# Kernel tuning notes

Hardware: AMD Instinct MI355X
Metric: run time of the kernel (lower is better)

Reference implementation:

```python
import jax, jax.numpy as jnp
import numpy as np

B, C, H, W = 16, 64, 128, 128
BN_EPS = 1e-5


def setup_inputs() -> dict:
    key = jax.random.key(0)
    ks = jax.random.split(key, 8)
    inp = {
        "x1": jax.random.normal(ks[0], (B, C, H, W), dtype=jnp.float32),
        "x2": jax.random.normal(ks[1], (B, C, H, W), dtype=jnp.float32),
        "rssi1": jax.random.normal(ks[2], (B, C, H, W), dtype=jnp.float32),
        "rssi2": jax.random.normal(ks[3], (B, C, H, W), dtype=jnp.float32),
        # 1x1 conv weights == per-pixel channel matmul; trunc_normal(std=0.02) approximated by normal*0.02
        "q_w": jax.random.normal(ks[4], (C, C), dtype=jnp.float32) * 0.02,
        "q_b": jnp.zeros((C,), dtype=jnp.float32),
        "k_w": jax.random.normal(ks[5], (C, C), dtype=jnp.float32) * 0.02,
        "k_b": jnp.zeros((C,), dtype=jnp.float32),
        "v_w": jax.random.normal(ks[6], (C, C), dtype=jnp.float32) * 0.02,
        "v_b": jnp.zeros((C,), dtype=jnp.float32),
        "bn_gamma": jnp.ones((C,), dtype=jnp.float32),
        "bn_beta": jnp.zeros((C,), dtype=jnp.float32),
    }
    return inp


def _proj(w, b, x):
    # 1x1 Conv2d: contract channel dim
    return jnp.einsum('oc,bchw->bohw', w, x) + b[None, :, None, None]


def _branch(q_w, q_b, k_w, k_b, v_w, v_b, rssi, x):
    q = _proj(q_w, q_b, rssi)            # [B,C,H,W]
    k = _proj(k_w, k_b, x)               # [B,C,H,W]
    v = _proj(v_w, v_b, x)               # [B,C,H,W]
    scale = 1.0 / jnp.sqrt(jnp.asarray(k.shape[-2], dtype=q.dtype))
    # matmul over trailing dims: [B,C,H,W] @ [B,C,W,H] -> [B,C,H,H]
    score = jax.nn.softmax(jnp.einsum('bchw,bcgw->bchg', q, k) * scale, axis=-1)
    return jnp.einsum('bchg,bcgw->bchw', score, v)  # [B,C,H,W]


def reference(x1, x2, rssi1, rssi2, q_w, q_b, k_w, k_b, v_w, v_b, bn_gamma, bn_beta):
    csi1 = _branch(q_w, q_b, k_w, k_b, v_w, v_b, rssi1, x1)
    csi2 = _branch(q_w, q_b, k_w, k_b, v_w, v_b, rssi2, x2)
    fused = csi1 + csi2
    # BatchNorm2d (training mode -> batch statistics over B,H,W), then ReLU
    mean = jnp.mean(fused, axis=(0, 2, 3), keepdims=True)
    var = jnp.var(fused, axis=(0, 2, 3), keepdims=True)
    g = bn_gamma[None, :, None, None]
    b = bn_beta[None, :, None, None]
    normed = (fused - mean) * jax.lax.rsqrt(var + BN_EPS) * g + b
    return jax.nn.relu(normed)
```

## Files before the change

### kernel.cpp

```cpp
#include <hip/hip_runtime.h>

#define HW 16384
#define NE 16777216ull

typedef short bf16x8 __attribute__((ext_vector_type(8)));
typedef _Float16 f16x8 __attribute__((ext_vector_type(8)));
typedef float f32x4  __attribute__((ext_vector_type(4)));

__device__ __forceinline__ unsigned short f2bf(float f) {
    unsigned int u = __float_as_uint(f);
    unsigned int r = (u + 0x7FFFu + ((u >> 16) & 1u)) >> 16;
    return (unsigned short)r;
}

__global__ __launch_bounds__(256)
void proj_mfma_kernel(const float* __restrict__ in,
                      const float* __restrict__ w1, const float* __restrict__ b1,
                      unsigned short* __restrict__ out1,
                      const float* __restrict__ w2, const float* __restrict__ b2,
                      unsigned short* __restrict__ out2,
                      float* __restrict__ stats) {
    __shared__ __align__(16) _Float16 xT[256 * 64];
    unsigned short* obuf = reinterpret_cast<unsigned short*>(xT);
    int tid = threadIdx.x;
    if (stats != nullptr && blockIdx.x == 0 && tid < 128) stats[tid] = 0.f;
    int pbase = blockIdx.x * 256;
    int b = pbase >> 14;
    int hw0 = pbase & 16383;
    const float* inb = in + (size_t)b * (64 * HW);

    {
        int n = tid;
        int swz = n & 7;
        const float* colp = inb + hw0 + n;
#pragma unroll
        for (int kc = 0; kc < 8; ++kc) {
            f16x8 ev;
#pragma unroll
            for (int j = 0; j < 8; ++j)
                ev[j] = (_Float16)colp[(kc * 8 + j) * HW];
            *reinterpret_cast<f16x8*>(&xT[n * 64 + ((kc ^ swz) * 8)]) = ev;
        }
    }

    int lane = tid & 63;
    int wv = tid >> 6;
    int quad = lane >> 4;
    int m16 = lane & 15;
    int mb = wv * 16;
    int sw = m16 & 7;
    int hasw2 = (w2 != nullptr);

    f16x8 a1[2], a2[2];
    float bias1[4], bias2[4];
#pragma unroll
    for (int ks = 0; ks < 2; ++ks) {
        const float* wr = w1 + (mb + m16) * 64 + (ks * 4 + quad) * 8;
        f16x8 ev;
#pragma unroll
        for (int j = 0; j < 8; ++j) ev[j] = (_Float16)wr[j];
        a1[ks] = ev;
    }
#pragma unroll
    for (int r = 0; r < 4; ++r) bias1[r] = b1[mb + quad * 4 + r];
    if (hasw2) {
#pragma unroll
        for (int ks = 0; ks < 2; ++ks) {
            const float* wr = w2 + (mb + m16) * 64 + (ks * 4 + quad) * 8;
            f16x8 ev;
#pragma unroll
            for (int j = 0; j < 8; ++j) ev[j] = (_Float16)wr[j];
            a2[ks] = ev;
        }
#pragma unroll
        for (int r = 0; r < 4; ++r) bias2[r] = b2[mb + quad * 4 + r];
    }
    __syncthreads();

    unsigned short* o1 = out1 + (size_t)b * (64 * HW);
    unsigned short* o2 = hasw2 ? (out2 + (size_t)b * (64 * HW)) : out1;

    unsigned int pk1[32], pk2[32];
#pragma unroll
    for (int nt = 0; nt < 16; ++nt) {
        int row = nt * 16 + m16;
        f16x8 bF0 = *reinterpret_cast<const f16x8*>(&xT[row * 64 + ((quad ^ sw) * 8)]);
        f16x8 bF1 = *reinterpret_cast<const f16x8*>(&xT[row * 64 + (((4 + quad) ^ sw) * 8)]);
        f32x4 acc1 = {bias1[0], bias1[1], bias1[2], bias1[3]};
        acc1 = __builtin_amdgcn_mfma_f32_16x16x32_f16(a1[0], bF0, acc1, 0, 0, 0);
        acc1 = __builtin_amdgcn_mfma_f32_16x16x32_f16(a1[1], bF1, acc1, 0, 0, 0);
        pk1[nt * 2 + 0] = (unsigned int)f2bf(acc1[0]) | ((unsigned int)f2bf(acc1[1]) << 16);
        pk1[nt * 2 + 1] = (unsigned int)f2bf(acc1[2]) | ((unsigned int)f2bf(acc1[3]) << 16);
        if (hasw2) {
            f32x4 acc2 = {bias2[0], bias2[1], bias2[2], bias2[3]};
            acc2 = __builtin_amdgcn_mfma_f32_16x16x32_f16(a2[0], bF0, acc2, 0, 0, 0);
            acc2 = __builtin_amdgcn_mfma_f32_16x16x32_f16(a2[1], bF1, acc2, 0, 0, 0);
            pk2[nt * 2 + 0] = (unsigned int)f2bf(acc2[0]) | ((unsigned int)f2bf(acc2[1]) << 16);
            pk2[nt * 2 + 1] = (unsigned int)f2bf(acc2[2]) | ((unsigned int)f2bf(acc2[3]) << 16);
        }
    }
    __syncthreads();

#pragma unroll
    for (int nt = 0; nt < 16; ++nt)
#pragma unroll
        for (int r = 0; r < 4; ++r) {
            int row = mb + quad * 4 + r;
            int col = nt * 16 + m16;
            unsigned int v = pk1[nt * 2 + (r >> 1)];
            unsigned short e = (r & 1) ? (unsigned short)(v >> 16) : (unsigned short)(v & 0xffff);
            obuf[row * 256 + (((col >> 3) ^ (row & 7)) * 8) + (col & 7)] = e;
        }
    __syncthreads();
#pragma unroll
    for (int k = 0; k < 8; ++k) {
        int c = k * 256 + tid;
        int row = c >> 5;
        int cg = c & 31;
        uint4 v = *reinterpret_cast<const uint4*>(&obuf[row * 256 + ((cg ^ (row & 7)) * 8)]);
        *reinterpret_cast<uint4*>(&o1[(size_t)row * HW + hw0 + cg * 8]) = v;
    }

    if (hasw2) {
        __syncthreads();
#pragma unroll
        for (int nt = 0; nt < 16; ++nt)
#pragma unroll
            for (int r = 0; r < 4; ++r) {
                int row = mb + quad * 4 + r;
                int col = nt * 16 + m16;
                unsigned int v = pk2[nt * 2 + (r >> 1)];
                unsigned short e = (r & 1) ? (unsigned short)(v >> 16) : (unsigned short)(v & 0xffff);
                obuf[row * 256 + (((col >> 3) ^ (row & 7)) * 8) + (col & 7)] = e;
            }
        __syncthreads();
#pragma unroll
        for (int k = 0; k < 8; ++k) {
            int c = k * 256 + tid;
            int row = c >> 5;
            int cg = c & 31;
            uint4 v = *reinterpret_cast<const uint4*>(&obuf[row * 256 + ((cg ^ (row & 7)) * 8)]);
            *reinterpret_cast<uint4*>(&o2[(size_t)row * HW + hw0 + cg * 8]) = v;
        }
    }
}

__global__ __launch_bounds__(512, 4)
void attn_kernel(const unsigned short* __restrict__ Q, const unsigned short* __restrict__ K,
                 const unsigned short* __restrict__ V, float* __restrict__ io,
                 float* __restrict__ stats, int accumulate) {
    __shared__ short bufA[16384];
    __shared__ short bufB[16384];
    int bc = blockIdx.x;
    size_t base = (size_t)bc * HW;
    int tid = threadIdx.x;
    int lane = tid & 63;
    int wv = tid >> 6;
    int quad = lane >> 4;
    int m16 = lane & 15;

    uint4 vreg[4];
    {
        int g0 = tid >> 4;
        int w0 = (tid & 15) * 8;
#pragma unroll
        for (int i = 0; i < 4; ++i)
            vreg[i] = *(const uint4*)(V + base + (size_t)(g0 + 32 * i) * 128 + w0);
    }

    {
        int r0 = tid >> 4;
        int c0 = tid & 15;
#pragma unroll
        for (int i = 0; i < 4; ++i) {
            int r = r0 + 32 * i;
            uint4 q = *(const uint4*)(Q + base + (size_t)r * 128 + c0 * 8);
            uint4 k = *(const uint4*)(K + base + (size_t)r * 128 + c0 * 8);
            int ch = c0 ^ (r & 7);
            *reinterpret_cast<uint4*>(&bufA[r * 128 + ch * 8]) = q;
            *reinterpret_cast<uint4*>(&bufB[r * 128 + ch * 8]) = k;
        }
    }
    __syncthreads();

    int rowA = wv * 16 + m16;
    int sw = m16 & 7;
    bf16x8 aF[4];
#pragma unroll
    for (int ks = 0; ks < 4; ++ks) {
        int ch = (ks * 4 + quad) ^ sw;
        aF[ks] = *reinterpret_cast<const bf16x8*>(&bufA[rowA * 128 + ch * 8]);
    }
    f32x4 sacc[8];
#pragma unroll
    for (int n = 0; n < 8; ++n) {
        f32x4 acc = {0.f, 0.f, 0.f, 0.f};
        int rowB = n * 16 + m16;
#pragma unroll
        for (int ks = 0; ks < 4; ++ks) {
            int ch = (ks * 4 + quad) ^ sw;
            bf16x8 bF = *reinterpret_cast<const bf16x8*>(&bufB[rowB * 128 + ch * 8]);
            acc = __builtin_amdgcn_mfma_f32_16x16x32_bf16(aF[ks], bF, acc, 0, 0, 0);
        }
        sacc[n] = acc;
    }

    const float scale = 0.08838834764831845f;
    float mx[4] = {-3.4e38f, -3.4e38f, -3.4e38f, -3.4e38f};
#pragma unroll
    for (int n = 0; n < 8; ++n)
#pragma unroll
        for (int r = 0; r < 4; ++r) {
            sacc[n][r] *= scale;
            mx[r] = fmaxf(mx[r], sacc[n][r]);
        }
#pragma unroll
    for (int mask = 8; mask >= 1; mask >>= 1)
#pragma unroll
        for (int r = 0; r < 4; ++r) mx[r] = fmaxf(mx[r], __shfl_xor(mx[r], mask));
    float sum[4] = {0.f, 0.f, 0.f, 0.f};
#pragma unroll
    for (int n = 0; n < 8; ++n)
#pragma unroll
        for (int r = 0; r < 4; ++r) {
            float e = __expf(sacc[n][r] - mx[r]);
            sacc[n][r] = e;
            sum[r] += e;
        }
#pragma unroll
    for (int mask = 8; mask >= 1; mask >>= 1)
#pragma unroll
        for (int r = 0; r < 4; ++r) sum[r] += __shfl_xor(sum[r], mask);
    float inv[4];
#pragma unroll
    for (int r = 0; r < 4; ++r) inv[r] = 1.0f / sum[r];

#pragma unroll
    for (int n = 0; n < 8; ++n)
#pragma unroll
        for (int r = 0; r < 4; ++r) {
            int row = wv * 16 + quad * 4 + r;
            int col = n * 16 + m16;
            int pos = row * 128 + (((col >> 3) ^ (row & 7)) * 8) + (col & 7);
            bufA[pos] = (short)f2bf(sacc[n][r] * inv[r]);
        }

    __syncthreads();

    float iopre[8][4];
    if (accumulate) {
#pragma unroll
        for (int n = 0; n < 8; ++n)
#pragma unroll
            for (int r = 0; r < 4; ++r)
                iopre[n][r] = io[base + (wv * 16 + quad * 4 + r) * 128 + n * 16 + m16];
    }

    {
        int g0 = tid >> 4;
        int w0 = (tid & 15) * 8;
#pragma unroll
        for (int i = 0; i < 4; ++i) {
            int g = g0 + 32 * i;
            unsigned short e[8];
            *(uint4*)e = vreg[i];
#pragma unroll
            for (int jj = 0; jj < 8; ++jj) {
                int j = jj ^ (tid & 7);
                int w = w0 + j;
                int pos = w * 128 + (((g >> 3) ^ (w & 7)) * 8) + (g & 7);
                bufB[pos] = (short)e[j];
            }
        }
    }
    __syncthreads();

#pragma unroll
    for (int ks = 0; ks < 4; ++ks) {
        int ch = (ks * 4 + quad) ^ sw;
        aF[ks] = *reinterpret_cast<const bf16x8*>(&bufA[rowA * 128 + ch * 8]);
    }
    f32x4 oacc[8];
#pragma unroll
    for (int n = 0; n < 8; ++n) {
        f32x4 acc = {0.f, 0.f, 0.f, 0.f};
        int rowB = n * 16 + m16;
#pragma unroll
        for (int ks = 0; ks < 4; ++ks) {
            int ch = (ks * 4 + quad) ^ sw;
            bf16x8 bF = *reinterpret_cast<const bf16x8*>(&bufB[rowB * 128 + ch * 8]);
            acc = __builtin_amdgcn_mfma_f32_16x16x32_bf16(aF[ks], bF, acc, 0, 0, 0);
        }
        oacc[n] = acc;
    }

    if (!accumulate) {
#pragma unroll
        for (int n = 0; n < 8; ++n)
#pragma unroll
            for (int r = 0; r < 4; ++r) {
                int row = wv * 16 + quad * 4 + r;
                int col = n * 16 + m16;
                io[base + row * 128 + col] = oacc[n][r];
            }
    } else {
        float lsum = 0.f, lsq = 0.f;
#pragma unroll
        for (int n = 0; n < 8; ++n)
#pragma unroll
            for (int r = 0; r < 4; ++r) {
                int row = wv * 16 + quad * 4 + r;
                int col = n * 16 + m16;
                size_t idx = base + row * 128 + col;
                float f = iopre[n][r] + oacc[n][r];
                io[idx] = f;
                lsum += f;
                lsq += f * f;
            }
#pragma unroll
        for (int mask = 32; mask >= 1; mask >>= 1) {
            lsum += __shfl_xor(lsum, mask);
            lsq  += __shfl_xor(lsq,  mask);
        }
        if (lane == 0) {
            int c = bc & 63;
            atomicAdd(&stats[c], lsum);
            atomicAdd(&stats[64 + c], lsq);
        }
    }
}

__global__ __launch_bounds__(256)
void bn_relu_kernel(float* __restrict__ io, const float* __restrict__ stats,
                    const float* __restrict__ gamma, const float* __restrict__ beta) {
    int idx = blockIdx.x * 256 + threadIdx.x;
    int e = idx << 2;
    int c = (e >> 14) & 63;
    const float invN = 1.0f / 262144.0f;
    float mean = stats[c] * invN;
    float var = stats[64 + c] * invN - mean * mean;
    float k = rsqrtf(var + 1e-5f) * gamma[c];
    float bb = beta[c] - mean * k;
    float4 f = reinterpret_cast<const float4*>(io)[idx];
    float4 o;
    o.x = fmaxf(f.x * k + bb, 0.f);
    o.y = fmaxf(f.y * k + bb, 0.f);
    o.z = fmaxf(f.z * k + bb, 0.f);
    o.w = fmaxf(f.w * k + bb, 0.f);
    reinterpret_cast<float4*>(io)[idx] = o;
}

extern "C" void kernel_launch(void* const* d_in, const int* in_sizes, int n_in,
                              void* d_out, int out_size, void* d_ws, size_t ws_size,
                              hipStream_t stream) {
    const float* x1 = (const float*)d_in[0];
    const float* x2 = (const float*)d_in[1];
    const float* rssi1 = (const float*)d_in[2];
    const float* rssi2 = (const float*)d_in[3];
    const float* qw = (const float*)d_in[4];
    const float* qb = (const float*)d_in[5];
    const float* kw = (const float*)d_in[6];
    const float* kb = (const float*)d_in[7];
    const float* vw = (const float*)d_in[8];
    const float* vb = (const float*)d_in[9];
    const float* gamma = (const float*)d_in[10];
    const float* beta = (const float*)d_in[11];

    float* stats = (float*)d_ws;
    unsigned short* Q = (unsigned short*)((char*)d_ws + 512);
    unsigned short* K = Q + NE;
    unsigned short* V = K + NE;
    float* io = (float*)d_out;

    proj_mfma_kernel<<<1024, 256, 0, stream>>>(rssi1, qw, qb, Q,
                                               nullptr, nullptr, nullptr, stats);
    proj_mfma_kernel<<<1024, 256, 0, stream>>>(x1, kw, kb, K, vw, vb, V, nullptr);
    attn_kernel<<<1024, 512, 0, stream>>>(Q, K, V, io, stats, 0);

    proj_mfma_kernel<<<1024, 256, 0, stream>>>(rssi2, qw, qb, Q,
                                               nullptr, nullptr, nullptr, nullptr);
    proj_mfma_kernel<<<1024, 256, 0, stream>>>(x2, kw, kb, K, vw, vb, V, nullptr);
    attn_kernel<<<1024, 512, 0, stream>>>(Q, K, V, io, stats, 1);

    bn_relu_kernel<<<16384, 256, 0, stream>>>(io, stats, gamma, beta);
}
```

Before: 443.5 us.

## Fuse both branches into single projection and attention launches

Merges the four projection launches into one grid that picks its job from the block index. When the workspace is large enough, the two attention passes become one kernel that computes both branches and accumulates them in registers. This removes the read-modify-write of the fp32 output between branches and cuts launch count. Q fragments are now loaded straight from global memory instead of staged through shared memory. The cost is a larger workspace, more register pressure in the attention kernel, and extra synchronisation inside it.

```diff
diff --git a/kernel.cpp b/kernel.cpp
--- a/kernel.cpp
+++ b/kernel.cpp
@@ -14,17 +14,30 @@
 }
 
 __global__ __launch_bounds__(256)
-void proj_mfma_kernel(const float* __restrict__ in,
-                      const float* __restrict__ w1, const float* __restrict__ b1,
-                      unsigned short* __restrict__ out1,
-                      const float* __restrict__ w2, const float* __restrict__ b2,
-                      unsigned short* __restrict__ out2,
+void proj_mfma_kernel(const float* __restrict__ rA, const float* __restrict__ xA,
+                      const float* __restrict__ rB, const float* __restrict__ xB,
+                      const float* __restrict__ qw, const float* __restrict__ qb,
+                      const float* __restrict__ kw, const float* __restrict__ kb,
+                      const float* __restrict__ vw, const float* __restrict__ vb,
+                      unsigned short* __restrict__ QA, unsigned short* __restrict__ KA,
+                      unsigned short* __restrict__ VA,
+                      unsigned short* __restrict__ QB, unsigned short* __restrict__ KB,
+                      unsigned short* __restrict__ VB,
                       float* __restrict__ stats) {
     __shared__ __align__(16) _Float16 xT[256 * 64];
     unsigned short* obuf = reinterpret_cast<unsigned short*>(xT);
     int tid = threadIdx.x;
     if (stats != nullptr && blockIdx.x == 0 && tid < 128) stats[tid] = 0.f;
-    int pbase = blockIdx.x * 256;
+
+    int job = blockIdx.x >> 10;
+    const float *in, *w1, *b1, *w2 = nullptr, *b2 = nullptr;
+    unsigned short *o1, *o2 = nullptr;
+    if (job == 0)      { in = rA; w1 = qw; b1 = qb; o1 = QA; }
+    else if (job == 1) { in = xA; w1 = kw; b1 = kb; o1 = KA; w2 = vw; b2 = vb; o2 = VA; }
+    else if (job == 2) { in = rB; w1 = qw; b1 = qb; o1 = QB; }
+    else               { in = xB; w1 = kw; b1 = kb; o1 = KB; w2 = vw; b2 = vb; o2 = VB; }
+
+    int pbase = (blockIdx.x & 1023) * 256;
     int b = pbase >> 14;
     int hw0 = pbase & 16383;
     const float* inb = in + (size_t)b * (64 * HW);
@@ -77,8 +90,8 @@
     }
     __syncthreads();
 
-    unsigned short* o1 = out1 + (size_t)b * (64 * HW);
-    unsigned short* o2 = hasw2 ? (out2 + (size_t)b * (64 * HW)) : out1;
+    unsigned short* o1b = o1 + (size_t)b * (64 * HW);
+    unsigned short* o2b = hasw2 ? (o2 + (size_t)b * (64 * HW)) : o1b;
 
     unsigned int pk1[32], pk2[32];
 #pragma unroll
@@ -118,7 +131,7 @@
         int row = c >> 5;
         int cg = c & 31;
         uint4 v = *reinterpret_cast<const uint4*>(&obuf[row * 256 + ((cg ^ (row & 7)) * 8)]);
-        *reinterpret_cast<uint4*>(&o1[(size_t)row * HW + hw0 + cg * 8]) = v;
+        *reinterpret_cast<uint4*>(&o1b[(size_t)row * HW + hw0 + cg * 8]) = v;
     }
 
     if (hasw2) {
@@ -140,16 +153,18 @@
             int row = c >> 5;
             int cg = c & 31;
             uint4 v = *reinterpret_cast<const uint4*>(&obuf[row * 256 + ((cg ^ (row & 7)) * 8)]);
-            *reinterpret_cast<uint4*>(&o2[(size_t)row * HW + hw0 + cg * 8]) = v;
+            *reinterpret_cast<uint4*>(&o2b[(size_t)row * HW + hw0 + cg * 8]) = v;
         }
     }
 }
 
 __global__ __launch_bounds__(512, 4)
-void attn_kernel(const unsigned short* __restrict__ Q, const unsigned short* __restrict__ K,
-                 const unsigned short* __restrict__ V, float* __restrict__ io,
-                 float* __restrict__ stats, int accumulate) {
-    __shared__ short bufA[16384];
+void attn_kernel(const unsigned short* __restrict__ Q1, const unsigned short* __restrict__ K1,
+                 const unsigned short* __restrict__ V1,
+                 const unsigned short* __restrict__ Q2, const unsigned short* __restrict__ K2,
+                 const unsigned short* __restrict__ V2,
+                 float* __restrict__ io, float* __restrict__ stats, int mode) {
+    __shared__ short bufP[16384];
     __shared__ short bufB[16384];
     int bc = blockIdx.x;
     size_t base = (size_t)bc * HW;
@@ -158,39 +173,33 @@
     int wv = tid >> 6;
     int quad = lane >> 4;
     int m16 = lane & 15;
-
-    uint4 vreg[4];
-    {
-        int g0 = tid >> 4;
-        int w0 = (tid & 15) * 8;
-#pragma unroll
-        for (int i = 0; i < 4; ++i)
-            vreg[i] = *(const uint4*)(V + base + (size_t)(g0 + 32 * i) * 128 + w0);
-    }
-
-    {
-        int r0 = tid >> 4;
-        int c0 = tid & 15;
-#pragma unroll
-        for (int i = 0; i < 4; ++i) {
-            int r = r0 + 32 * i;
-            uint4 q = *(const uint4*)(Q + base + (size_t)r * 128 + c0 * 8);
-            uint4 k = *(const uint4*)(K + base + (size_t)r * 128 + c0 * 8);
-            int ch = c0 ^ (r & 7);
-            *reinterpret_cast<uint4*>(&bufA[r * 128 + ch * 8]) = q;
-            *reinterpret_cast<uint4*>(&bufB[r * 128 + ch * 8]) = k;
-        }
-    }
-    __syncthreads();
-
     int rowA = wv * 16 + m16;
     int sw = m16 & 7;
+    int g0 = tid >> 4;
+    int c0 = tid & 15;
+    int w0 = c0 * 8;
+
+    uint4 vreg[4];
+#pragma unroll
+    for (int i = 0; i < 4; ++i)
+        vreg[i] = *(const uint4*)(V1 + base + (size_t)(g0 + 32 * i) * 128 + w0);
+    uint4 kst[4];
+#pragma unroll
+    for (int i = 0; i < 4; ++i)
+        kst[i] = *(const uint4*)(K1 + base + (size_t)(g0 + 32 * i) * 128 + w0);
     bf16x8 aF[4];
 #pragma unroll
-    for (int ks = 0; ks < 4; ++ks) {
-        int ch = (ks * 4 + quad) ^ sw;
-        aF[ks] = *reinterpret_cast<const bf16x8*>(&bufA[rowA * 128 + ch * 8]);
-    }
+    for (int ks = 0; ks < 4; ++ks)
+        aF[ks] = *reinterpret_cast<const bf16x8*>(Q1 + base + (size_t)rowA * 128 + (ks * 4 + quad) * 8);
+
+#pragma unroll
+    for (int i = 0; i < 4; ++i) {
+        int r = g0 + 32 * i;
+        int ch = c0 ^ (r & 7);
+        *reinterpret_cast<uint4*>(&bufB[r * 128 + ch * 8]) = kst[i];
+    }
+    __syncthreads();
+
     f32x4 sacc[8];
 #pragma unroll
     for (int n = 0; n < 8; ++n) {
@@ -206,34 +215,37 @@
     }
 
     const float scale = 0.08838834764831845f;
-    float mx[4] = {-3.4e38f, -3.4e38f, -3.4e38f, -3.4e38f};
-#pragma unroll
-    for (int n = 0; n < 8; ++n)
-#pragma unroll
-        for (int r = 0; r < 4; ++r) {
-            sacc[n][r] *= scale;
-            mx[r] = fmaxf(mx[r], sacc[n][r]);
-        }
-#pragma unroll
-    for (int mask = 8; mask >= 1; mask >>= 1)
-#pragma unroll
-        for (int r = 0; r < 4; ++r) mx[r] = fmaxf(mx[r], __shfl_xor(mx[r], mask));
-    float sum[4] = {0.f, 0.f, 0.f, 0.f};
-#pragma unroll
-    for (int n = 0; n < 8; ++n)
-#pragma unroll
-        for (int r = 0; r < 4; ++r) {
-            float e = __expf(sacc[n][r] - mx[r]);
-            sacc[n][r] = e;
-            sum[r] += e;
-        }
-#pragma unroll
-    for (int mask = 8; mask >= 1; mask >>= 1)
-#pragma unroll
-        for (int r = 0; r < 4; ++r) sum[r] += __shfl_xor(sum[r], mask);
-    float inv[4];
-#pragma unroll
-    for (int r = 0; r < 4; ++r) inv[r] = 1.0f / sum[r];
+    {
+        float mx[4] = {-3.4e38f, -3.4e38f, -3.4e38f, -3.4e38f};
+#pragma unroll
+        for (int n = 0; n < 8; ++n)
+#pragma unroll
+            for (int r = 0; r < 4; ++r) {
+                sacc[n][r] *= scale;
+                mx[r] = fmaxf(mx[r], sacc[n][r]);
+            }
+#pragma unroll
+        for (int mask = 8; mask >= 1; mask >>= 1)
+#pragma unroll
+            for (int r = 0; r < 4; ++r) mx[r] = fmaxf(mx[r], __shfl_xor(mx[r], mask));
+        float sum[4] = {0.f, 0.f, 0.f, 0.f};
+#pragma unroll
+        for (int n = 0; n < 8; ++n)
+#pragma unroll
+            for (int r = 0; r < 4; ++r) {
+                float e = __expf(sacc[n][r] - mx[r]);
+                sacc[n][r] = e;
+                sum[r] += e;
+            }
+#pragma unroll
+        for (int mask = 8; mask >= 1; mask >>= 1)
+#pragma unroll
+            for (int r = 0; r < 4; ++r) sum[r] += __shfl_xor(sum[r], mask);
+#pragma unroll
+        for (int n = 0; n < 8; ++n)
+#pragma unroll
+            for (int r = 0; r < 4; ++r) sacc[n][r] *= 1.0f / sum[r];
+    }
 
 #pragma unroll
     for (int n = 0; n < 8; ++n)
@@ -242,23 +254,22 @@
             int row = wv * 16 + quad * 4 + r;
             int col = n * 16 + m16;
             int pos = row * 128 + (((col >> 3) ^ (row & 7)) * 8) + (col & 7);
-            bufA[pos] = (short)f2bf(sacc[n][r] * inv[r]);
+            bufP[pos] = (short)f2bf(sacc[n][r]);
         }
 
     __syncthreads();
 
-    float iopre[8][4];
-    if (accumulate) {
-#pragma unroll
-        for (int n = 0; n < 8; ++n)
-#pragma unroll
-            for (int r = 0; r < 4; ++r)
-                iopre[n][r] = io[base + (wv * 16 + quad * 4 + r) * 128 + n * 16 + m16];
+    bf16x8 qF2[4];
+    if (mode == 2) {
+#pragma unroll
+        for (int i = 0; i < 4; ++i)
+            kst[i] = *(const uint4*)(K2 + base + (size_t)(g0 + 32 * i) * 128 + w0);
+#pragma unroll
+        for (int ks = 0; ks < 4; ++ks)
+            qF2[ks] = *reinterpret_cast<const bf16x8*>(Q2 + base + (size_t)rowA * 128 + (ks * 4 + quad) * 8);
     }
 
     {
-        int g0 = tid >> 4;
-        int w0 = (tid & 15) * 8;
 #pragma unroll
         for (int i = 0; i < 4; ++i) {
             int g = g0 + 32 * i;
@@ -273,12 +284,17 @@
             }
         }
     }
+    if (mode == 2) {
+#pragma unroll
+        for (int i = 0; i < 4; ++i)
+            vreg[i] = *(const uint4*)(V2 + base + (size_t)(g0 + 32 * i) * 128 + w0);
+    }
     __syncthreads();
 
 #pragma unroll
     for (int ks = 0; ks < 4; ++ks) {
         int ch = (ks * 4 + quad) ^ sw;
-        aF[ks] = *reinterpret_cast<const bf16x8*>(&bufA[rowA * 128 + ch * 8]);
+        aF[ks] = *reinterpret_cast<const bf16x8*>(&bufP[rowA * 128 + ch * 8]);
     }
     f32x4 oacc[8];
 #pragma unroll
@@ -294,7 +310,107 @@
         oacc[n] = acc;
     }
 
-    if (!accumulate) {
+    if (mode == 2) {
+        __syncthreads();
+#pragma unroll
+        for (int i = 0; i < 4; ++i) {
+            int r = g0 + 32 * i;
+            int ch = c0 ^ (r & 7);
+            *reinterpret_cast<uint4*>(&bufB[r * 128 + ch * 8]) = kst[i];
+        }
+        __syncthreads();
+
+#pragma unroll
+        for (int n = 0; n < 8; ++n) {
+            f32x4 acc = {0.f, 0.f, 0.f, 0.f};
+            int rowB = n * 16 + m16;
+#pragma unroll
+            for (int ks = 0; ks < 4; ++ks) {
+                int ch = (ks * 4 + quad) ^ sw;
+                bf16x8 bF = *reinterpret_cast<const bf16x8*>(&bufB[rowB * 128 + ch * 8]);
+                acc = __builtin_amdgcn_mfma_f32_16x16x32_bf16(qF2[ks], bF, acc, 0, 0, 0);
+            }
+            sacc[n] = acc;
+        }
+
+        {
+            float mx[4] = {-3.4e38f, -3.4e38f, -3.4e38f, -3.4e38f};
+#pragma unroll
+            for (int n = 0; n < 8; ++n)
+#pragma unroll
+                for (int r = 0; r < 4; ++r) {
+                    sacc[n][r] *= scale;
+                    mx[r] = fmaxf(mx[r], sacc[n][r]);
+                }
+#pragma unroll
+            for (int mask = 8; mask >= 1; mask >>= 1)
+#pragma unroll
+                for (int r = 0; r < 4; ++r) mx[r] = fmaxf(mx[r], __shfl_xor(mx[r], mask));
+            float sum[4] = {0.f, 0.f, 0.f, 0.f};
+#pragma unroll
+            for (int n = 0; n < 8; ++n)
+#pragma unroll
+                for (int r = 0; r < 4; ++r) {
+                    float e = __expf(sacc[n][r] - mx[r]);
+                    sacc[n][r] = e;
+                    sum[r] += e;
+                }
+#pragma unroll
+            for (int mask = 8; mask >= 1; mask >>= 1)
+#pragma unroll
+                for (int r = 0; r < 4; ++r) sum[r] += __shfl_xor(sum[r], mask);
+#pragma unroll
+            for (int n = 0; n < 8; ++n)
+#pragma unroll
+                for (int r = 0; r < 4; ++r) sacc[n][r] *= 1.0f / sum[r];
+        }
+
+#pragma unroll
+        for (int n = 0; n < 8; ++n)
+#pragma unroll
+            for (int r = 0; r < 4; ++r) {
+                int row = wv * 16 + quad * 4 + r;
+                int col = n * 16 + m16;
+                int pos = row * 128 + (((col >> 3) ^ (row & 7)) * 8) + (col & 7);
+                bufP[pos] = (short)f2bf(sacc[n][r]);
+            }
+        __syncthreads();
+
+#pragma unroll
+        for (int i = 0; i < 4; ++i) {
+            int g = g0 + 32 * i;
+            unsigned short e[8];
+            *(uint4*)e = vreg[i];
+#pragma unroll
+            for (int jj = 0; jj < 8; ++jj) {
+                int j = jj ^ (tid & 7);
+                int w = w0 + j;
+                int pos = w * 128 + (((g >> 3) ^ (w & 7)) * 8) + (g & 7);
+                bufB[pos] = (short)e[j];
+            }
+        }
+        __syncthreads();
+
+#pragma unroll
+        for (int ks = 0; ks < 4; ++ks) {
+            int ch = (ks * 4 + quad) ^ sw;
+            aF[ks] = *reinterpret_cast<const bf16x8*>(&bufP[rowA * 128 + ch * 8]);
+        }
+#pragma unroll
+        for (int n = 0; n < 8; ++n) {
+            f32x4 acc = oacc[n];
+            int rowB = n * 16 + m16;
+#pragma unroll
+            for (int ks = 0; ks < 4; ++ks) {
+                int ch = (ks * 4 + quad) ^ sw;
+                bf16x8 bF = *reinterpret_cast<const bf16x8*>(&bufB[rowB * 128 + ch * 8]);
+                acc = __builtin_amdgcn_mfma_f32_16x16x32_bf16(aF[ks], bF, acc, 0, 0, 0);
+            }
+            oacc[n] = acc;
+        }
+    }
+
+    if (mode == 0) {
 #pragma unroll
         for (int n = 0; n < 8; ++n)
 #pragma unroll
@@ -312,7 +428,8 @@
                 int row = wv * 16 + quad * 4 + r;
                 int col = n * 16 + m16;
                 size_t idx = base + row * 128 + col;
-                float f = iopre[n][r] + oacc[n][r];
+                float f = oacc[n][r];
+                if (mode == 1) f += io[idx];
                 io[idx] = f;
                 lsum += f;
                 lsq += f * f;
@@ -367,20 +484,31 @@
     const float* beta = (const float*)d_in[11];
 
     float* stats = (float*)d_ws;
-    unsigned short* Q = (unsigned short*)((char*)d_ws + 512);
-    unsigned short* K = Q + NE;
-    unsigned short* V = K + NE;
+    unsigned short* Q1 = (unsigned short*)((char*)d_ws + 512);
+    unsigned short* K1 = Q1 + NE;
+    unsigned short* V1 = K1 + NE;
     float* io = (float*)d_out;
 
-    proj_mfma_kernel<<<1024, 256, 0, stream>>>(rssi1, qw, qb, Q,
-                                               nullptr, nullptr, nullptr, stats);
-    proj_mfma_kernel<<<1024, 256, 0, stream>>>(x1, kw, kb, K, vw, vb, V, nullptr);
-    attn_kernel<<<1024, 512, 0, stream>>>(Q, K, V, io, stats, 0);
-
-    proj_mfma_kernel<<<1024, 256, 0, stream>>>(rssi2, qw, qb, Q,
-                                               nullptr, nullptr, nullptr, nullptr);
-    proj_mfma_kernel<<<1024, 256, 0, stream>>>(x2, kw, kb, K, vw, vb, V, nullptr);
-    attn_kernel<<<1024, 512, 0, stream>>>(Q, K, V, io, stats, 1);
+    const size_t need_dual = 512 + 6 * NE * 2;
+
+    if (ws_size >= need_dual) {
+        unsigned short* Q2 = V1 + NE;
+        unsigned short* K2 = Q2 + NE;
+        unsigned short* V2 = K2 + NE;
+        proj_mfma_kernel<<<4096, 256, 0, stream>>>(rssi1, x1, rssi2, x2,
+                                                   qw, qb, kw, kb, vw, vb,
+                                                   Q1, K1, V1, Q2, K2, V2, stats);
+        attn_kernel<<<1024, 512, 0, stream>>>(Q1, K1, V1, Q2, K2, V2, io, stats, 2);
+    } else {
+        proj_mfma_kernel<<<2048, 256, 0, stream>>>(rssi1, x1, nullptr, nullptr,
+                                                   qw, qb, kw, kb, vw, vb,
+                                                   Q1, K1, V1, nullptr, nullptr, nullptr, stats);
+        attn_kernel<<<1024, 512, 0, stream>>>(Q1, K1, V1, nullptr, nullptr, nullptr, io, stats, 0);
+        proj_mfma_kernel<<<2048, 256, 0, stream>>>(rssi2, x2, nullptr, nullptr,
+                                                   qw, qb, kw, kb, vw, vb,
+                                                   Q1, K1, V1, nullptr, nullptr, nullptr, nullptr);
+        attn_kernel<<<1024, 512, 0, stream>>>(Q1, K1, V1, nullptr, nullptr, nullptr, io, stats, 1);
+    }
 
     bn_relu_kernel<<<16384, 256, 0, stream>>>(io, stats, gamma, beta);
 }
```

Measured after the change: 446.4 us. Within noise of the previous version (+0.6%).
